# Kernel optimization log

Hardware: AMD Instinct MI355X
Metric: run time of the kernel (lower is better)

## Reference

```python
import jax, jax.numpy as jnp
import numpy as np

B, HQ, HKV, D = 32, 32, 8, 128
BLOCK_SIZE, MAX_BLOCKS = 16, 128
NUM_BLOCKS = B * MAX_BLOCKS
LMAX = MAX_BLOCKS * BLOCK_SIZE  # 2048 max context per sequence
ROPE_BASE = 10000.0


def _rope(x, pos):
    """Apply rotary embedding. x: [B, H, D], pos: [B] int positions."""
    half = D // 2
    inv_freq = 1.0 / (ROPE_BASE ** (jnp.arange(0, D, 2, dtype=jnp.float32) / D))  # [D/2]
    freqs = pos.astype(jnp.float32)[:, None] * inv_freq[None, :]  # [B, D/2]
    emb = jnp.concatenate([freqs, freqs], axis=-1)                # [B, D]
    cos = jnp.cos(emb)[:, None, :]  # [B, 1, D]
    sin = jnp.sin(emb)[:, None, :]
    x1, x2 = x[..., :half], x[..., half:]
    rotated = jnp.concatenate([-x2, x1], axis=-1)
    return x * cos + rotated * sin


def setup_inputs() -> dict:
    key = jax.random.key(0)
    ks = jax.random.split(key, 6)
    query = jax.random.normal(ks[0], (B, HQ, D), jnp.float32)
    new_k = jax.random.normal(ks[1], (B, HKV, D), jnp.float32)
    new_v = jax.random.normal(ks[2], (B, HKV, D), jnp.float32)
    k_cache = jax.random.normal(ks[3], (NUM_BLOCKS, BLOCK_SIZE, HKV, D), jnp.float32)
    v_cache = jax.random.normal(ks[4], (NUM_BLOCKS, BLOCK_SIZE, HKV, D), jnp.float32)
    # each sequence owns a disjoint contiguous range of blocks
    block_table = jnp.arange(B * MAX_BLOCKS, dtype=jnp.int32).reshape(B, MAX_BLOCKS)
    context_lens = jax.random.randint(ks[5], (B,), 1, LMAX - 1).astype(jnp.int32)
    return dict(query=query, new_k=new_k, new_v=new_v, k_cache=k_cache,
                v_cache=v_cache, block_table=block_table, context_lens=context_lens)


def reference(query, new_k, new_v, k_cache, v_cache, block_table, context_lens):
    scale = 1.0 / D ** 0.5
    pos = context_lens  # new token position for each sequence, [B]

    # RoPE on the decode-step query and key (seq_len == 1 per sequence)
    q = _rope(query, pos)      # [B, HQ, D]
    k_new = _rope(new_k, pos)  # [B, HKV, D]

    # flatten paged cache to [NUM_BLOCKS*BLOCK_SIZE, HKV, D]
    kc = k_cache.reshape(-1, HKV, D)
    vc = v_cache.reshape(-1, HKV, D)

    # paged KV-cache append: slot = block_table[b, pos//bs]*bs + pos%bs
    blk_new = jnp.take_along_axis(block_table, (pos // BLOCK_SIZE)[:, None], axis=1)[:, 0]
    slot = blk_new * BLOCK_SIZE + pos % BLOCK_SIZE  # [B]
    kc = kc.at[slot].set(k_new)
    vc = vc.at[slot].set(new_v)

    # gather per-sequence K/V via block table: [B, LMAX, HKV, D]
    p = jnp.arange(LMAX, dtype=jnp.int32)
    blks = block_table[:, p // BLOCK_SIZE]                 # [B, LMAX]
    idx = blks * BLOCK_SIZE + (p % BLOCK_SIZE)[None, :]    # [B, LMAX]
    keys = kc[idx]
    vals = vc[idx]

    # GQA attention over valid context (lengths = context_lens + 1 after append)
    lens = pos + 1
    g = HQ // HKV
    qg = q.reshape(B, HKV, g, D)
    scores = jnp.einsum('bkgd,blkd->bkgl', qg, keys) * scale  # [B, HKV, g, LMAX]
    mask = p[None, :] < lens[:, None]  # [B, LMAX]
    scores = jnp.where(mask[:, None, None, :], scores, -jnp.inf)
    w = jax.nn.softmax(scores, axis=-1)
    out = jnp.einsum('bkgl,blkd->bkgd', w, vals)
    return out.reshape(B, HQ, D)
```

## Files before the change

### kernel.cpp

```cpp
#include <hip/hip_runtime.h>
#include <math.h>

#define BATCH 32
#define HQ 32
#define HKV 8
#define DHEAD 128
#define BS 16
#define MAXB 128
#define G 4
#define LMAX 2048
#define NBKV (BATCH * HKV)
#define BLKF (BS * HKV * DHEAD)

#define SCALE_LOG2E 0.12752740305928724f

typedef float v2f __attribute__((ext_vector_type(2)));

__device__ __forceinline__ v2f pk_fma(v2f a, v2f b, v2f c) {
    v2f d;
    asm("v_pk_fma_f32 %0, %1, %2, %3" : "=v"(d) : "v"(a), "v"(b), "v"(c));
    return d;
}
__device__ __forceinline__ v2f pk_mul(v2f a, v2f b) {
    v2f d;
    asm("v_pk_mul_f32 %0, %1, %2" : "=v"(d) : "v"(a), "v"(b));
    return d;
}
__device__ __forceinline__ float fexp2(float x) {
    float r;
    asm("v_exp_f32 %0, %1" : "=v"(r) : "v"(x));
    return r;
}

#define ROR4(N, x0, x1, x2, x3)                                                   \
    asm("s_nop 1\n\t"                                                             \
        "v_add_f32_dpp %0, %0, %0 row_ror:" #N " row_mask:0xf bank_mask:0xf\n\t"  \
        "v_add_f32_dpp %1, %1, %1 row_ror:" #N " row_mask:0xf bank_mask:0xf\n\t"  \
        "v_add_f32_dpp %2, %2, %2 row_ror:" #N " row_mask:0xf bank_mask:0xf\n\t"  \
        "v_add_f32_dpp %3, %3, %3 row_ror:" #N " row_mask:0xf bank_mask:0xf"      \
        : "+v"(x0), "+v"(x1), "+v"(x2), "+v"(x3))

template <int PP>
__global__ __launch_bounds__(512) void paged_attn_chunk(
    const float* __restrict__ query,
    const float* __restrict__ k_cache,
    const float* __restrict__ v_cache,
    const int*   __restrict__ block_table,
    const int*   __restrict__ context_lens,
    float*       __restrict__ wsacc,
    float*       __restrict__ wsl)
{
    constexpr int NCHK = LMAX / PP;
    constexpr int NCB  = PP / 16;
    constexpr int NIT  = PP / 2;

    const int c = blockIdx.x % NCHK;
    const int b = blockIdx.x / NCHK;
    const int pos = context_lens[b];
    const int c0  = c * PP;
    if (c0 >= pos) return;

    const int tid  = threadIdx.x;
    const int w    = tid >> 6;
    const int lane = tid & 63;
    const int half = lane >> 5;
    const int l5   = lane & 31;

    __shared__ float s_q[HQ * DHEAD];
    __shared__ float s_cos[64], s_sin[64];

    if (tid < 64) {
        float invf = exp2f((float)tid * -0.20762050593046014f);
        float ang  = (float)pos * invf;
        s_cos[tid] = cosf(ang);
        s_sin[tid] = sinf(ang);
    }
    __syncthreads();

    for (int idx = tid; idx < HQ * DHEAD; idx += 512) {
        int head = idx >> 7, d = idx & 127;
        const float* qp = query + ((size_t)b * HQ + head) * DHEAD;
        float x = qp[d], r;
        if (d < 64) r = x * s_cos[d]      - qp[d + 64] * s_sin[d];
        else        r = x * s_cos[d - 64] + qp[d - 64] * s_sin[d - 64];
        s_q[idx] = r * SCALE_LOG2E;
    }
    __syncthreads();

    v2f q2[G][2];
    #pragma unroll
    for (int h = 0; h < G; ++h) {
        float4 t4 = *(const float4*)&s_q[(w * G + h) * DHEAD + l5 * 4];
        q2[h][0] = v2f{t4.x, t4.y};
        q2[h][1] = v2f{t4.z, t4.w};
    }

    const float* kbase[NCB];
    const float* vbase[NCB];
    const int vofs = half * (HKV * DHEAD) + w * DHEAD + l5 * 4;
    #pragma unroll
    for (int i = 0; i < NCB; ++i) {
        int bt = __builtin_amdgcn_readfirstlane(block_table[b * MAXB + c * NCB + i]);
        kbase[i] = k_cache + (size_t)bt * BLKF + vofs;
        vbase[i] = v_cache + (size_t)bt * BLKF + vofs;
    }

    v2f acc[G][2];
    float lsum[G];
    #pragma unroll
    for (int h = 0; h < G; ++h) {
        lsum[h] = 0.f;
        acc[h][0] = v2f{0.f, 0.f};
        acc[h][1] = v2f{0.f, 0.f};
    }

#define LOADIT(K, V, IT)                                                        \
    do {                                                                        \
        K = *(const float4*)(kbase[(IT) >> 3] + ((IT) & 7) * (2 * HKV * DHEAD));\
        V = *(const float4*)(vbase[(IT) >> 3] + ((IT) & 7) * (2 * HKV * DHEAD));\
    } while (0)

    float4 K0, V0, K1, V1;
    LOADIT(K0, V0, 0);

    #pragma unroll
    for (int IT = 0; IT < NIT; ++IT) {
        if (IT + 1 < NIT) LOADIT(K1, V1, IT + 1);
        const int pi = c0 + 2 * IT + half;
        v2f k01 = v2f{K0.x, K0.y}, k23 = v2f{K0.z, K0.w};
        v2f d0 = pk_fma(q2[0][1], k23, pk_mul(q2[0][0], k01));
        v2f d1 = pk_fma(q2[1][1], k23, pk_mul(q2[1][0], k01));
        v2f d2 = pk_fma(q2[2][1], k23, pk_mul(q2[2][0], k01));
        v2f d3 = pk_fma(q2[3][1], k23, pk_mul(q2[3][0], k01));
        float dt0 = d0.x + d0.y, dt1 = d1.x + d1.y;
        float dt2 = d2.x + d2.y, dt3 = d3.x + d3.y;
        ROR4(8, dt0, dt1, dt2, dt3);
        ROR4(4, dt0, dt1, dt2, dt3);
        ROR4(2, dt0, dt1, dt2, dt3);
        ROR4(1, dt0, dt1, dt2, dt3);
        dt0 += __shfl_xor(dt0, 16, 64);
        dt1 += __shfl_xor(dt1, 16, 64);
        dt2 += __shfl_xor(dt2, 16, 64);
        dt3 += __shfl_xor(dt3, 16, 64);
        const bool act = pi < pos;
        float wg0 = act ? fexp2(dt0) : 0.f;
        float wg1 = act ? fexp2(dt1) : 0.f;
        float wg2 = act ? fexp2(dt2) : 0.f;
        float wg3 = act ? fexp2(dt3) : 0.f;
        lsum[0] += wg0; lsum[1] += wg1; lsum[2] += wg2; lsum[3] += wg3;
        v2f u01 = v2f{V0.x, V0.y}, u23 = v2f{V0.z, V0.w};
        acc[0][0] = pk_fma(v2f{wg0, wg0}, u01, acc[0][0]);
        acc[0][1] = pk_fma(v2f{wg0, wg0}, u23, acc[0][1]);
        acc[1][0] = pk_fma(v2f{wg1, wg1}, u01, acc[1][0]);
        acc[1][1] = pk_fma(v2f{wg1, wg1}, u23, acc[1][1]);
        acc[2][0] = pk_fma(v2f{wg2, wg2}, u01, acc[2][0]);
        acc[2][1] = pk_fma(v2f{wg2, wg2}, u23, acc[2][1]);
        acc[3][0] = pk_fma(v2f{wg3, wg3}, u01, acc[3][0]);
        acc[3][1] = pk_fma(v2f{wg3, wg3}, u23, acc[3][1]);
        K0 = K1; V0 = V1;
    }
#undef LOADIT

    #pragma unroll
    for (int h = 0; h < G; ++h) {
        lsum[h] += __shfl_xor(lsum[h], 32, 64);
        #pragma unroll
        for (int j = 0; j < 2; ++j) {
            float ax = acc[h][j].x, ay = acc[h][j].y;
            ax += __shfl_xor(ax, 32, 64);
            ay += __shfl_xor(ay, 32, 64);
            acc[h][j] = v2f{ax, ay};
        }
    }

    if (half == 0) {
        const size_t slot = ((size_t)b * NCHK + c) * HKV + w;
        #pragma unroll
        for (int h = 0; h < G; ++h) {
            float4 o4 = make_float4(acc[h][0].x, acc[h][0].y,
                                    acc[h][1].x, acc[h][1].y);
            *(float4*)&wsacc[slot * (G * DHEAD) + h * DHEAD + l5 * 4] = o4;
        }
        if (l5 == 0) {
            #pragma unroll
            for (int h = 0; h < G; ++h) wsl[slot * G + h] = lsum[h];
        }
    }
}

template <int PP>
__global__ __launch_bounds__(512) void paged_attn_combine(
    const float* __restrict__ query,
    const float* __restrict__ new_k,
    const float* __restrict__ new_v,
    const int*   __restrict__ context_lens,
    const float* __restrict__ wsacc,
    const float* __restrict__ wsl,
    float*       __restrict__ out)
{
    constexpr int NCHK = LMAX / PP;
    const int bkv = blockIdx.x;
    const int kv  = bkv & 7;
    const int b   = bkv >> 3;
    const int t   = threadIdx.x;
    const int h   = t >> 7;
    const int d   = t & 127;
    const int wv  = t >> 6;

    __shared__ float s_cos[64], s_sin[64], s_kn[DHEAD], s_ps[8];

    const int pos = context_lens[b];
    if (t < 64) {
        float invf = exp2f((float)t * -0.20762050593046014f);
        float ang  = (float)pos * invf;
        s_cos[t] = cosf(ang);
        s_sin[t] = sinf(ang);
    }
    __syncthreads();
    if (t < DHEAD) {
        const float* kp = new_k + ((size_t)b * HKV + kv) * DHEAD;
        float x = kp[t], r;
        if (t < 64) r = x * s_cos[t]      - kp[t + 64] * s_sin[t];
        else        r = x * s_cos[t - 64] + kp[t - 64] * s_sin[t - 64];
        s_kn[t] = r;
    }
    __syncthreads();

    float rq;
    {
        const float* qp = query + ((size_t)b * HQ + kv * G + h) * DHEAD;
        float x = qp[d];
        if (d < 64) rq = x * s_cos[d]      - qp[d + 64] * s_sin[d];
        else        rq = x * s_cos[d - 64] + qp[d - 64] * s_sin[d - 64];
        rq *= SCALE_LOG2E;
    }
    float part = rq * s_kn[d];
    #pragma unroll
    for (int off = 1; off < 64; off <<= 1) part += __shfl_xor(part, off, 64);
    if ((t & 63) == 0) s_ps[wv] = part;
    __syncthreads();

    const float wnew = fexp2(s_ps[2 * h] + s_ps[2 * h + 1]);

    const int ncc = (pos + PP - 1) / PP;

    float asum = 0.f, lsum = 0.f;
    for (int cc = 0; cc < ncc; cc++) {
        const size_t slot = ((size_t)b * NCHK + cc) * HKV + kv;
        asum += wsacc[slot * (G * DHEAD) + t];
        lsum += wsl[slot * G + h];
    }
    const float vnew = new_v[((size_t)b * HKV + kv) * DHEAD + d];
    out[((size_t)b * HQ + kv * G + h) * DHEAD + d] =
        (asum + wnew * vnew) / (lsum + wnew);
}

extern "C" void kernel_launch(void* const* d_in, const int* in_sizes, int n_in,
                              void* d_out, int out_size, void* d_ws, size_t ws_size,
                              hipStream_t stream) {
    const float* query        = (const float*)d_in[0];
    const float* new_k        = (const float*)d_in[1];
    const float* new_v        = (const float*)d_in[2];
    const float* k_cache      = (const float*)d_in[3];
    const float* v_cache      = (const float*)d_in[4];
    const int*   block_table  = (const int*)d_in[5];
    const int*   context_lens = (const int*)d_in[6];
    float* out = (float*)d_out;

    const size_t slots32 = (size_t)BATCH * (LMAX / 32) * HKV;
    const size_t need32  = slots32 * (G * DHEAD + G) * sizeof(float);

    if (ws_size >= need32) {
        constexpr int PP = 32;
        float* wsacc = (float*)d_ws;
        float* wsl   = wsacc + (size_t)BATCH * (LMAX / PP) * HKV * G * DHEAD;
        paged_attn_chunk<PP><<<dim3(BATCH * (LMAX / PP)), dim3(512), 0, stream>>>(
            query, k_cache, v_cache, block_table, context_lens, wsacc, wsl);
        paged_attn_combine<PP><<<dim3(NBKV), dim3(512), 0, stream>>>(
            query, new_k, new_v, context_lens, wsacc, wsl, out);
    } else {
        constexpr int PP = 64;
        float* wsacc = (float*)d_ws;
        float* wsl   = wsacc + (size_t)BATCH * (LMAX / PP) * HKV * G * DHEAD;
        paged_attn_chunk<PP><<<dim3(BATCH * (LMAX / PP)), dim3(512), 0, stream>>>(
            query, k_cache, v_cache, block_table, context_lens, wsacc, wsl);
        paged_attn_combine<PP><<<dim3(NBKV), dim3(512), 0, stream>>>(
            query, new_k, new_v, context_lens, wsacc, wsl, out);
    }
}
```

Before: 88.22 us.

## Restructure paged attention into prep, 128-token chunks with in-block reduction, and combine

Adds a separate prep kernel that applies RoPE to the query and writes it pre-scaled to workspace, so the chunk kernel no longer redoes it per block. The chunk kernel now handles 128 tokens per block: each warp reads a contiguous 32-token slice for two KV heads at once, with double-buffered loads, and the four warp groups are summed through shared memory before one write per chunk. The goal is fewer blocks, coalesced block-contiguous reads, less workspace traffic, and a shorter combine loop. The costs are an extra kernel launch, serialized shared-memory reduction barriers, and more registers per thread.

```diff
diff --git a/kernel.cpp b/kernel.cpp
--- a/kernel.cpp
+++ b/kernel.cpp
@@ -9,6 +9,9 @@
 #define MAXB 128
 #define G 4
 #define LMAX 2048
+#define CHUNK 128
+#define NCH (LMAX / CHUNK)
+#define NSLOT (BATCH * NCH)
 #define NBKV (BATCH * HKV)
 #define BLKF (BS * HKV * DHEAD)
 
@@ -40,35 +43,18 @@
         "v_add_f32_dpp %3, %3, %3 row_ror:" #N " row_mask:0xf bank_mask:0xf"      \
         : "+v"(x0), "+v"(x1), "+v"(x2), "+v"(x3))
 
-template <int PP>
-__global__ __launch_bounds__(512) void paged_attn_chunk(
+__global__ __launch_bounds__(128) void paged_attn_prep(
     const float* __restrict__ query,
-    const float* __restrict__ k_cache,
-    const float* __restrict__ v_cache,
-    const int*   __restrict__ block_table,
     const int*   __restrict__ context_lens,
-    float*       __restrict__ wsacc,
-    float*       __restrict__ wsl)
+    float* __restrict__ qs)
 {
-    constexpr int NCHK = LMAX / PP;
-    constexpr int NCB  = PP / 16;
-    constexpr int NIT  = PP / 2;
-
-    const int c = blockIdx.x % NCHK;
-    const int b = blockIdx.x / NCHK;
+    const int bkv = blockIdx.x;
+    const int kv  = bkv & 7;
+    const int b   = bkv >> 3;
+    const int tid = threadIdx.x;
+
+    __shared__ float s_cos[64], s_sin[64];
     const int pos = context_lens[b];
-    const int c0  = c * PP;
-    if (c0 >= pos) return;
-
-    const int tid  = threadIdx.x;
-    const int w    = tid >> 6;
-    const int lane = tid & 63;
-    const int half = lane >> 5;
-    const int l5   = lane & 31;
-
-    __shared__ float s_q[HQ * DHEAD];
-    __shared__ float s_cos[64], s_sin[64];
-
     if (tid < 64) {
         float invf = exp2f((float)tid * -0.20762050593046014f);
         float ang  = (float)pos * invf;
@@ -77,118 +63,196 @@
     }
     __syncthreads();
 
-    for (int idx = tid; idx < HQ * DHEAD; idx += 512) {
-        int head = idx >> 7, d = idx & 127;
-        const float* qp = query + ((size_t)b * HQ + head) * DHEAD;
+    for (int idx = tid; idx < G * DHEAD; idx += 128) {
+        int h = idx >> 7, d = idx & 127;
+        const float* qp = query + ((size_t)b * HQ + kv * G + h) * DHEAD;
         float x = qp[d], r;
         if (d < 64) r = x * s_cos[d]      - qp[d + 64] * s_sin[d];
         else        r = x * s_cos[d - 64] + qp[d - 64] * s_sin[d - 64];
-        s_q[idx] = r * SCALE_LOG2E;
-    }
-    __syncthreads();
-
-    v2f q2[G][2];
+        qs[(size_t)bkv * (G * DHEAD) + idx] = r * SCALE_LOG2E;
+    }
+}
+
+__global__ __launch_bounds__(512) void paged_attn_chunk(
+    const float* __restrict__ k_cache,
+    const float* __restrict__ v_cache,
+    const int*   __restrict__ block_table,
+    const int*   __restrict__ context_lens,
+    const float* __restrict__ qs,
+    float*       __restrict__ wsacc,
+    float*       __restrict__ wsl)
+{
+    const int c = blockIdx.x & (NCH - 1);
+    const int b = blockIdx.x >> 4;
+    const int pos = context_lens[b];
+    const int c0  = c * CHUNK;
+    if (c0 >= pos) return;
+
+    const int tid  = threadIdx.x;
+    const int w    = tid >> 6;
+    const int g    = w >> 1;
+    const int half = w & 1;
+    const int lane = tid & 63;
+    const int l32  = lane & 31;
+    const int hi   = lane >> 5;
+
+    __shared__ float s_acc[HKV][G][DHEAD];
+    __shared__ float s_l[HKV][G];
+
+    v2f q2[2][G][2];
     #pragma unroll
-    for (int h = 0; h < G; ++h) {
-        float4 t4 = *(const float4*)&s_q[(w * G + h) * DHEAD + l5 * 4];
-        q2[h][0] = v2f{t4.x, t4.y};
-        q2[h][1] = v2f{t4.z, t4.w};
-    }
-
-    const float* kbase[NCB];
-    const float* vbase[NCB];
-    const int vofs = half * (HKV * DHEAD) + w * DHEAD + l5 * 4;
-    #pragma unroll
-    for (int i = 0; i < NCB; ++i) {
-        int bt = __builtin_amdgcn_readfirstlane(block_table[b * MAXB + c * NCB + i]);
-        kbase[i] = k_cache + (size_t)bt * BLKF + vofs;
-        vbase[i] = v_cache + (size_t)bt * BLKF + vofs;
-    }
-
-    v2f acc[G][2];
-    float lsum[G];
-    #pragma unroll
-    for (int h = 0; h < G; ++h) {
-        lsum[h] = 0.f;
-        acc[h][0] = v2f{0.f, 0.f};
-        acc[h][1] = v2f{0.f, 0.f};
-    }
-
-#define LOADIT(K, V, IT)                                                        \
-    do {                                                                        \
-        K = *(const float4*)(kbase[(IT) >> 3] + ((IT) & 7) * (2 * HKV * DHEAD));\
-        V = *(const float4*)(vbase[(IT) >> 3] + ((IT) & 7) * (2 * HKV * DHEAD));\
-    } while (0)
-
-    float4 K0, V0, K1, V1;
-    LOADIT(K0, V0, 0);
-
-    #pragma unroll
-    for (int IT = 0; IT < NIT; ++IT) {
-        if (IT + 1 < NIT) LOADIT(K1, V1, IT + 1);
-        const int pi = c0 + 2 * IT + half;
-        v2f k01 = v2f{K0.x, K0.y}, k23 = v2f{K0.z, K0.w};
-        v2f d0 = pk_fma(q2[0][1], k23, pk_mul(q2[0][0], k01));
-        v2f d1 = pk_fma(q2[1][1], k23, pk_mul(q2[1][0], k01));
-        v2f d2 = pk_fma(q2[2][1], k23, pk_mul(q2[2][0], k01));
-        v2f d3 = pk_fma(q2[3][1], k23, pk_mul(q2[3][0], k01));
-        float dt0 = d0.x + d0.y, dt1 = d1.x + d1.y;
-        float dt2 = d2.x + d2.y, dt3 = d3.x + d3.y;
-        ROR4(8, dt0, dt1, dt2, dt3);
-        ROR4(4, dt0, dt1, dt2, dt3);
-        ROR4(2, dt0, dt1, dt2, dt3);
-        ROR4(1, dt0, dt1, dt2, dt3);
-        dt0 += __shfl_xor(dt0, 16, 64);
-        dt1 += __shfl_xor(dt1, 16, 64);
-        dt2 += __shfl_xor(dt2, 16, 64);
-        dt3 += __shfl_xor(dt3, 16, 64);
-        const bool act = pi < pos;
-        float wg0 = act ? fexp2(dt0) : 0.f;
-        float wg1 = act ? fexp2(dt1) : 0.f;
-        float wg2 = act ? fexp2(dt2) : 0.f;
-        float wg3 = act ? fexp2(dt3) : 0.f;
-        lsum[0] += wg0; lsum[1] += wg1; lsum[2] += wg2; lsum[3] += wg3;
-        v2f u01 = v2f{V0.x, V0.y}, u23 = v2f{V0.z, V0.w};
-        acc[0][0] = pk_fma(v2f{wg0, wg0}, u01, acc[0][0]);
-        acc[0][1] = pk_fma(v2f{wg0, wg0}, u23, acc[0][1]);
-        acc[1][0] = pk_fma(v2f{wg1, wg1}, u01, acc[1][0]);
-        acc[1][1] = pk_fma(v2f{wg1, wg1}, u23, acc[1][1]);
-        acc[2][0] = pk_fma(v2f{wg2, wg2}, u01, acc[2][0]);
-        acc[2][1] = pk_fma(v2f{wg2, wg2}, u23, acc[2][1]);
-        acc[3][0] = pk_fma(v2f{wg3, wg3}, u01, acc[3][0]);
-        acc[3][1] = pk_fma(v2f{wg3, wg3}, u23, acc[3][1]);
-        K0 = K1; V0 = V1;
-    }
-#undef LOADIT
-
-    #pragma unroll
-    for (int h = 0; h < G; ++h) {
-        lsum[h] += __shfl_xor(lsum[h], 32, 64);
-        #pragma unroll
-        for (int j = 0; j < 2; ++j) {
-            float ax = acc[h][j].x, ay = acc[h][j].y;
-            ax += __shfl_xor(ax, 32, 64);
-            ay += __shfl_xor(ay, 32, 64);
-            acc[h][j] = v2f{ax, ay};
-        }
-    }
-
-    if (half == 0) {
-        const size_t slot = ((size_t)b * NCHK + c) * HKV + w;
+    for (int i = 0; i < 2; ++i) {
+        const int kv = half * 4 + 2 * i + hi;
         #pragma unroll
         for (int h = 0; h < G; ++h) {
-            float4 o4 = make_float4(acc[h][0].x, acc[h][0].y,
-                                    acc[h][1].x, acc[h][1].y);
-            *(float4*)&wsacc[slot * (G * DHEAD) + h * DHEAD + l5 * 4] = o4;
+            const float4 t4 = *(const float4*)
+                &qs[(((size_t)b * HKV + kv) * G + h) * DHEAD + 4 * l32];
+            q2[i][h][0] = v2f{t4.x, t4.y};
+            q2[i][h][1] = v2f{t4.z, t4.w};
         }
-        if (l5 == 0) {
+    }
+
+    v2f acc[2][G][2];
+    float lsum[2][G];
+    #pragma unroll
+    for (int i = 0; i < 2; ++i)
+        #pragma unroll
+        for (int h = 0; h < G; ++h) {
+            lsum[i][h] = 0.f;
+            acc[i][h][0] = v2f{0.f, 0.f};
+            acc[i][h][1] = v2f{0.f, 0.f};
+        }
+
+    const int pbase = c0 + g * 32;
+    if (pbase < pos) {
+        const int cbi = b * MAXB + (pbase >> 4);
+        const int bt0 = __builtin_amdgcn_readfirstlane(block_table[cbi]);
+        const int bt1 = __builtin_amdgcn_readfirstlane(block_table[cbi + 1]);
+
+        const int lofs = half * 512 + lane * 4;
+        const float* kb0 = k_cache + (size_t)bt0 * BLKF + lofs;
+        const float* kb1 = k_cache + (size_t)bt1 * BLKF + lofs;
+        const float* vb0 = v_cache + (size_t)bt0 * BLKF + lofs;
+        const float* vb1 = v_cache + (size_t)bt1 * BLKF + lofs;
+
+#define LOADP(S, P)                                                            \
+    do {                                                                       \
+        const float* kb_ = (P) < 16 ? kb0 : kb1;                               \
+        const float* vb_ = (P) < 16 ? vb0 : vb1;                               \
+        const int o_ = ((P) & 15) * 1024;                                      \
+        S[0] = *(const float4*)(kb_ + o_);            \
+        S[1] = *(const float4*)(kb_ + o_ + 256);      \
+        S[2] = *(const float4*)(vb_ + o_);                                     \
+        S[3] = *(const float4*)(vb_ + o_ + 256);                               \
+    } while (0)
+
+#define COMPP(S, P)                                                            \
+    do {                                                                       \
+        v2f kl0 = v2f{S[0].x, S[0].y}, kh0 = v2f{S[0].z, S[0].w};              \
+        v2f kl1 = v2f{S[1].x, S[1].y}, kh1 = v2f{S[1].z, S[1].w};              \
+        v2f e00 = pk_fma(q2[0][0][1], kh0, pk_mul(q2[0][0][0], kl0));          \
+        v2f e01 = pk_fma(q2[0][1][1], kh0, pk_mul(q2[0][1][0], kl0));          \
+        v2f e02 = pk_fma(q2[0][2][1], kh0, pk_mul(q2[0][2][0], kl0));          \
+        v2f e03 = pk_fma(q2[0][3][1], kh0, pk_mul(q2[0][3][0], kl0));          \
+        v2f e10 = pk_fma(q2[1][0][1], kh1, pk_mul(q2[1][0][0], kl1));          \
+        v2f e11 = pk_fma(q2[1][1][1], kh1, pk_mul(q2[1][1][0], kl1));          \
+        v2f e12 = pk_fma(q2[1][2][1], kh1, pk_mul(q2[1][2][0], kl1));          \
+        v2f e13 = pk_fma(q2[1][3][1], kh1, pk_mul(q2[1][3][0], kl1));          \
+        float d00 = e00.x + e00.y, d01 = e01.x + e01.y;                        \
+        float d02 = e02.x + e02.y, d03 = e03.x + e03.y;                        \
+        float d10 = e10.x + e10.y, d11 = e11.x + e11.y;                        \
+        float d12 = e12.x + e12.y, d13 = e13.x + e13.y;                        \
+        ROR4(8, d00, d01, d02, d03);  ROR4(8, d10, d11, d12, d13);             \
+        ROR4(4, d00, d01, d02, d03);  ROR4(4, d10, d11, d12, d13);             \
+        ROR4(2, d00, d01, d02, d03);  ROR4(2, d10, d11, d12, d13);             \
+        ROR4(1, d00, d01, d02, d03);  ROR4(1, d10, d11, d12, d13);             \
+        d00 += __shfl_xor(d00, 16, 64); d01 += __shfl_xor(d01, 16, 64);        \
+        d02 += __shfl_xor(d02, 16, 64); d03 += __shfl_xor(d03, 16, 64);        \
+        d10 += __shfl_xor(d10, 16, 64); d11 += __shfl_xor(d11, 16, 64);        \
+        d12 += __shfl_xor(d12, 16, 64); d13 += __shfl_xor(d13, 16, 64);        \
+        const bool act_ = (pbase + (P)) < pos;                                 \
+        float w00 = act_ ? fexp2(d00) : 0.f;                                   \
+        float w01 = act_ ? fexp2(d01) : 0.f;                                   \
+        float w02 = act_ ? fexp2(d02) : 0.f;                                   \
+        float w03 = act_ ? fexp2(d03) : 0.f;                                   \
+        float w10 = act_ ? fexp2(d10) : 0.f;                                   \
+        float w11 = act_ ? fexp2(d11) : 0.f;                                   \
+        float w12 = act_ ? fexp2(d12) : 0.f;                                   \
+        float w13 = act_ ? fexp2(d13) : 0.f;                                   \
+        lsum[0][0] += w00; lsum[0][1] += w01;                                  \
+        lsum[0][2] += w02; lsum[0][3] += w03;                                  \
+        lsum[1][0] += w10; lsum[1][1] += w11;                                  \
+        lsum[1][2] += w12; lsum[1][3] += w13;                                  \
+        v2f ul0 = v2f{S[2].x, S[2].y}, uh0 = v2f{S[2].z, S[2].w};              \
+        v2f ul1 = v2f{S[3].x, S[3].y}, uh1 = v2f{S[3].z, S[3].w};              \
+        acc[0][0][0] = pk_fma(v2f{w00, w00}, ul0, acc[0][0][0]);               \
+        acc[0][0][1] = pk_fma(v2f{w00, w00}, uh0, acc[0][0][1]);               \
+        acc[0][1][0] = pk_fma(v2f{w01, w01}, ul0, acc[0][1][0]);               \
+        acc[0][1][1] = pk_fma(v2f{w01, w01}, uh0, acc[0][1][1]);               \
+        acc[0][2][0] = pk_fma(v2f{w02, w02}, ul0, acc[0][2][0]);               \
+        acc[0][2][1] = pk_fma(v2f{w02, w02}, uh0, acc[0][2][1]);               \
+        acc[0][3][0] = pk_fma(v2f{w03, w03}, ul0, acc[0][3][0]);               \
+        acc[0][3][1] = pk_fma(v2f{w03, w03}, uh0, acc[0][3][1]);               \
+        acc[1][0][0] = pk_fma(v2f{w10, w10}, ul1, acc[1][0][0]);               \
+        acc[1][0][1] = pk_fma(v2f{w10, w10}, uh1, acc[1][0][1]);               \
+        acc[1][1][0] = pk_fma(v2f{w11, w11}, ul1, acc[1][1][0]);               \
+        acc[1][1][1] = pk_fma(v2f{w11, w11}, uh1, acc[1][1][1]);               \
+        acc[1][2][0] = pk_fma(v2f{w12, w12}, ul1, acc[1][2][0]);               \
+        acc[1][2][1] = pk_fma(v2f{w12, w12}, uh1, acc[1][2][1]);               \
+        acc[1][3][0] = pk_fma(v2f{w13, w13}, ul1, acc[1][3][0]);               \
+        acc[1][3][1] = pk_fma(v2f{w13, w13}, uh1, acc[1][3][1]);               \
+    } while (0)
+
+        float4 stA[4], stB[4];
+        LOADP(stA, 0);
+        #pragma unroll
+        for (int p = 0; p < 32; p += 2) {
+            LOADP(stB, p + 1);
+            COMPP(stA, p);
+            if (p + 2 < 32) LOADP(stA, p + 2);
+            COMPP(stB, p + 1);
+        }
+#undef LOADP
+#undef COMPP
+    }
+
+    #pragma unroll
+    for (int r = 0; r < 4; ++r) {
+        if (g == r) {
             #pragma unroll
-            for (int h = 0; h < G; ++h) wsl[slot * G + h] = lsum[h];
+            for (int i = 0; i < 2; ++i) {
+                const int kv = half * 4 + 2 * i + hi;
+                float* dst = &s_acc[kv][0][0];
+                #pragma unroll
+                for (int h = 0; h < G; ++h) {
+                    float* dp = dst + h * DHEAD + 4 * l32;
+                    if (r == 0) {
+                        dp[0] = acc[i][h][0].x; dp[1] = acc[i][h][0].y;
+                        dp[2] = acc[i][h][1].x; dp[3] = acc[i][h][1].y;
+                    } else {
+                        dp[0] += acc[i][h][0].x; dp[1] += acc[i][h][0].y;
+                        dp[2] += acc[i][h][1].x; dp[3] += acc[i][h][1].y;
+                    }
+                }
+                if (l32 == 0) {
+                    #pragma unroll
+                    for (int h = 0; h < G; ++h) {
+                        if (r == 0) s_l[kv][h]  = lsum[i][h];
+                        else        s_l[kv][h] += lsum[i][h];
+                    }
+                }
+            }
         }
-    }
-}
-
-template <int PP>
+        __syncthreads();
+    }
+
+    const size_t sbase = (size_t)blockIdx.x * (HKV * G * DHEAD);
+    for (int idx = tid; idx < HKV * G * DHEAD; idx += 512)
+        wsacc[sbase + idx] = (&s_acc[0][0][0])[idx];
+    if (tid < HKV * G)
+        wsl[(size_t)blockIdx.x * (HKV * G) + tid] = (&s_l[0][0])[tid];
+}
+
 __global__ __launch_bounds__(512) void paged_attn_combine(
     const float* __restrict__ query,
     const float* __restrict__ new_k,
@@ -198,7 +262,6 @@
     const float* __restrict__ wsl,
     float*       __restrict__ out)
 {
-    constexpr int NCHK = LMAX / PP;
     const int bkv = blockIdx.x;
     const int kv  = bkv & 7;
     const int b   = bkv >> 3;
@@ -242,13 +305,13 @@
 
     const float wnew = fexp2(s_ps[2 * h] + s_ps[2 * h + 1]);
 
-    const int ncc = (pos + PP - 1) / PP;
+    const int ncc = (pos + CHUNK - 1) >> 7;
 
     float asum = 0.f, lsum = 0.f;
     for (int cc = 0; cc < ncc; cc++) {
-        const size_t slot = ((size_t)b * NCHK + cc) * HKV + kv;
-        asum += wsacc[slot * (G * DHEAD) + t];
-        lsum += wsl[slot * G + h];
+        const size_t slot = (size_t)b * NCH + cc;
+        asum += wsacc[slot * (HKV * G * DHEAD) + kv * (G * DHEAD) + t];
+        lsum += wsl[slot * (HKV * G) + kv * G + h];
     }
     const float vnew = new_v[((size_t)b * HKV + kv) * DHEAD + d];
     out[((size_t)b * HQ + kv * G + h) * DHEAD + d] =
@@ -267,24 +330,14 @@
     const int*   context_lens = (const int*)d_in[6];
     float* out = (float*)d_out;
 
-    const size_t slots32 = (size_t)BATCH * (LMAX / 32) * HKV;
-    const size_t need32  = slots32 * (G * DHEAD + G) * sizeof(float);
-
-    if (ws_size >= need32) {
-        constexpr int PP = 32;
-        float* wsacc = (float*)d_ws;
-        float* wsl   = wsacc + (size_t)BATCH * (LMAX / PP) * HKV * G * DHEAD;
-        paged_attn_chunk<PP><<<dim3(BATCH * (LMAX / PP)), dim3(512), 0, stream>>>(
-            query, k_cache, v_cache, block_table, context_lens, wsacc, wsl);
-        paged_attn_combine<PP><<<dim3(NBKV), dim3(512), 0, stream>>>(
-            query, new_k, new_v, context_lens, wsacc, wsl, out);
-    } else {
-        constexpr int PP = 64;
-        float* wsacc = (float*)d_ws;
-        float* wsl   = wsacc + (size_t)BATCH * (LMAX / PP) * HKV * G * DHEAD;
-        paged_attn_chunk<PP><<<dim3(BATCH * (LMAX / PP)), dim3(512), 0, stream>>>(
-            query, k_cache, v_cache, block_table, context_lens, wsacc, wsl);
-        paged_attn_combine<PP><<<dim3(NBKV), dim3(512), 0, stream>>>(
-            query, new_k, new_v, context_lens, wsacc, wsl, out);
-    }
-}
+    float* wsacc = (float*)d_ws;
+    float* wsl   = wsacc + (size_t)NSLOT * HKV * G * DHEAD;
+    float* qs    = wsl + (size_t)NSLOT * HKV * G;
+
+    paged_attn_prep<<<dim3(NBKV), dim3(128), 0, stream>>>(
+        query, context_lens, qs);
+    paged_attn_chunk<<<dim3(NSLOT), dim3(512), 0, stream>>>(
+        k_cache, v_cache, block_table, context_lens, qs, wsacc, wsl);
+    paged_attn_combine<<<dim3(NBKV), dim3(512), 0, stream>>>(
+        query, new_k, new_v, context_lens, wsacc, wsl, out);
+}
```

Result: slower. 189.0 us (+114.2%).
